# Kernel tuning notes

Hardware: AMD Instinct MI355X
Metric: run time of the kernel (lower is better)

The kernel has to match this reference:

```python
import jax, jax.numpy as jnp
import numpy as np
from jax.scipy.special import digamma, gammaln, logsumexp

N, K, D = 262144, 256, 64
ALPHA = 1.0  # alphaDP
LOG2PI = float(np.log(2.0 * np.pi))


def setup_inputs() -> dict:
    key = jax.random.key(0)
    k1, k2, k3, k4 = jax.random.split(key, 4)
    x = jax.random.normal(k1, (N, D), jnp.float32)
    # variational params (perturbed from the module's init so grads are nontrivial)
    u = 1.0 + jax.random.uniform(k2, (K,), jnp.float32)
    v = 1.0 + jax.random.uniform(k3, (K,), jnp.float32)
    tau = jax.random.normal(k4, (K, D), jnp.float32)
    c = jnp.ones((K,), jnp.float32)
    n = jnp.full((K,), float(D), jnp.float32)   # must be > D-1
    B = jnp.ones((K, D), jnp.float32)
    # fixed prior hyper-parameters (buffers, per init_kwargs)
    tau0 = jnp.zeros((K, D), jnp.float32)
    c0 = jnp.ones((K,), jnp.float32)
    n0 = jnp.full((K,), float(D), jnp.float32)
    B0 = jnp.ones((K, D), jnp.float32)
    return dict(x=x, u=u, v=v, tau=tau, c=c, n=n, B=B,
                tau0=tau0, c0=c0, n0=n0, B0=B0)


def _dpmm_forward(x, u, v, tau, c, n, B, tau0, c0, n0, B0):
    # --- E[log pi_k] from stick-breaking Beta(u_k, v_k) posteriors ---
    dig_sum = digamma(u + v)
    elog_beta = digamma(u) - dig_sum            # (K,)
    elog_1mbeta = digamma(v) - dig_sum          # (K,)
    elog_pi = elog_beta + jnp.concatenate(
        [jnp.zeros((1,), elog_beta.dtype), jnp.cumsum(elog_1mbeta)[:-1]])

    # --- expected Gaussian log-likelihood under diagonal Normal-Wishart q ---
    Elam = n[:, None] / B                                        # (K, D) E[lambda]
    Eloglam = digamma(0.5 * n)[:, None] + jnp.log(2.0) - jnp.log(B)
    # quadratic form sum_d E[lam_kd](x_id - tau_kd)^2 via matmuls (no NxKxD tensor)
    quad = ((x * x) @ Elam.T
            - 2.0 * (x @ (Elam * tau).T)
            + jnp.sum(Elam * tau * tau, axis=-1)[None, :])       # (N, K)
    eloglik = 0.5 * (jnp.sum(Eloglam, axis=-1)[None, :]
                     - D * LOG2PI
                     - (D / c)[None, :]
                     - quad)                                     # (N, K)

    # --- responsibilities ---
    log_rho = elog_pi[None, :] + eloglik                         # (N, K)
    lse = logsumexp(log_rho, axis=-1)                            # (N,)
    pi = jnp.exp(log_rho - lse[:, None])                         # (N, K)

    # --- ELBO: sum_i r_ik (log_rho - log r) = sum_i logsumexp_i, minus KLs ---
    # KL(Beta(u,v) || Beta(1, alpha))
    kl_beta = jnp.sum(gammaln(u + v) - gammaln(u) - gammaln(v)
                      - (gammaln(1.0 + ALPHA) - gammaln(ALPHA))
                      + (u - 1.0) * elog_beta
                      + (v - ALPHA) * elog_1mbeta)
    # KL of diagonal Wishart (per-dim Gamma(n/2, rate=B/2))
    a, a0 = 0.5 * n[:, None], 0.5 * n0[:, None]
    b, b0 = 0.5 * B, 0.5 * B0
    kl_gam = ((a - a0) * digamma(a) - gammaln(a) + gammaln(a0)
              + a0 * (jnp.log(b) - jnp.log(b0)) + a * (b0 - b) / b)  # (K, D)
    # E_lambda KL of conditional Normal(tau, (c lambda)^-1)
    kl_norm = (0.5 * D * (c0 / c - 1.0 + jnp.log(c / c0))
               + 0.5 * c0 * jnp.sum((n[:, None] / B) * (tau - tau0) ** 2, axis=-1))

    elbo = jnp.sum(lse) - kl_beta - jnp.sum(kl_gam) - jnp.sum(kl_norm)
    return pi, elbo


def reference(x, u, v, tau, c, n, B, tau0, c0, n0, B0):
    return _dpmm_forward(x, u, v, tau, c, n, B, tau0, c0, n0, B0)
```

## Files before the change

kernel.cpp:

```cpp
#include <hip/hip_runtime.h>
#include <math.h>
#include <stdint.h>

#define NPTS 262144
#define KCL  256
#define DDIM 64
#define ALPHA_DP 1.0f

#define ROWS_PER_WAVE 32
#define WAVES_PER_BLK 8
#define ROWS_PER_BLK  (ROWS_PER_WAVE * WAVES_PER_BLK)
#define NBLK_MAIN     (NPTS / ROWS_PER_BLK)
#define NPART         (NPTS / ROWS_PER_WAVE)

#define OFF_ELOGPI 32768
#define OFF_BASE   33024
#define OFF_KLB    33280
#define OFF_KLP    33281
#define OFF_PART   33537

#define LN2_F    0.6931471805599453f
#define LOG2PI_F 1.8378770664093453f

typedef _Float16 f16x8  __attribute__((ext_vector_type(8)));
typedef float    f32x4  __attribute__((ext_vector_type(4)));
typedef float    f32x16 __attribute__((ext_vector_type(16)));

__device__ __forceinline__ float digamma_f(float x) {
  float r = 0.0f;
  while (x < 6.0f) { r -= 1.0f / x; x += 1.0f; }
  float inv  = 1.0f / x;
  float inv2 = inv * inv;
  return r + logf(x) - 0.5f * inv
       - inv2 * (0.083333333333333333f
         - inv2 * (0.008333333333333333f
           - inv2 * 0.003968253968253968f));
}

__global__ __launch_bounds__(64) void dpmm_prep(
    const float* __restrict__ u,   const float* __restrict__ v,
    const float* __restrict__ tau, const float* __restrict__ c,
    const float* __restrict__ n,   const float* __restrict__ B,
    const float* __restrict__ tau0, const float* __restrict__ c0,
    const float* __restrict__ n0,  const float* __restrict__ B0,
    float* __restrict__ ws) {
  const int tid = threadIdx.x;

  if (blockIdx.x == KCL) {
    float eb[4], e1b[4], klb[4];
    #pragma unroll
    for (int q = 0; q < 4; ++q) {
      int k = tid * 4 + q;
      float uk = u[k], vk = v[k];
      float ds = digamma_f(uk + vk);
      eb[q]  = digamma_f(uk) - ds;
      e1b[q] = digamma_f(vk) - ds;
      klb[q] = lgammaf(uk + vk) - lgammaf(uk) - lgammaf(vk)
             - (lgammaf(1.0f + ALPHA_DP) - lgammaf(ALPHA_DP))
             + (uk - 1.0f) * eb[q] + (vk - ALPHA_DP) * e1b[q];
    }
    float sum4 = e1b[0] + e1b[1] + e1b[2] + e1b[3];
    float sc = sum4;
    #pragma unroll
    for (int off = 1; off < 64; off <<= 1) {
      float vv = __shfl_up(sc, off, 64);
      if (tid >= off) sc += vv;
    }
    float pre = sc - sum4;
    ws[OFF_ELOGPI + 4 * tid + 0] = eb[0] + pre;  pre += e1b[0];
    ws[OFF_ELOGPI + 4 * tid + 1] = eb[1] + pre;  pre += e1b[1];
    ws[OFF_ELOGPI + 4 * tid + 2] = eb[2] + pre;  pre += e1b[2];
    ws[OFF_ELOGPI + 4 * tid + 3] = eb[3] + pre;
    float ks = klb[0] + klb[1] + klb[2] + klb[3];
    #pragma unroll
    for (int off = 32; off; off >>= 1) ks += __shfl_xor(ks, off, 64);
    if (tid == 0) ws[OFF_KLB] = ks;
    return;
  }

  const int k = blockIdx.x, d = tid;
  _Float16* Wp = (_Float16*)ws;

  float nk = n[k], ck = c[k], n0k = n0[k], c0k = c0[k];
  float Bkd = B[k * DDIM + d],   tkd  = tau[k * DDIM + d];
  float B0kd = B0[k * DDIM + d], t0kd = tau0[k * DDIM + d];
  float Elam = nk / Bkd;
  float wb = Elam * tkd;
  float wa = -0.5f * Elam;

  const int ct = k & 7, col = k >> 3;
  int   kks[2] = { d, 64 + d };
  float wvs[2] = { wb, wa };
  #pragma unroll
  for (int q = 0; q < 2; ++q) {
    int kk = kks[q]; float wq = wvs[q];
    int s = kk >> 4, rem = kk & 15, h = rem >> 3, e = rem & 7;
    int lanei = col + h * 32;
    _Float16 hi = (_Float16)wq, lo = (_Float16)(wq - (float)hi);
    Wp[( s * 8 + ct)     * 512 + lanei * 8 + e] = hi;
    Wp[(64 + s * 8 + ct) * 512 + lanei * 8 + e] = lo;
  }

  float a = 0.5f * nk, a0 = 0.5f * n0k;
  float dga = digamma_f(a);
  float lga = lgammaf(a), lga0 = lgammaf(a0);
  float b = 0.5f * Bkd, b0 = 0.5f * B0kd;
  float klg = (a - a0) * dga - lga + lga0
            + a0 * (logf(b) - logf(b0)) + a * (b0 - b) / b;
  float dt = tkd - t0kd;
  float knq = Elam * dt * dt;
  float negLogB = -logf(Bkd);
  float et2 = Elam * tkd * tkd;

  #pragma unroll
  for (int off = 32; off; off >>= 1) {
    klg     += __shfl_xor(klg, off, 64);
    knq     += __shfl_xor(knq, off, 64);
    negLogB += __shfl_xor(negLogB, off, 64);
    et2     += __shfl_xor(et2, off, 64);
  }
  if (d == 0) {
    float sumEloglam = (float)DDIM * (dga + LN2_F) + negLogB;
    ws[OFF_BASE + k] = 0.5f * (sumEloglam - (float)DDIM * LOG2PI_F
                               - (float)DDIM / ck - et2);
    float kln = 0.5f * (float)DDIM * (c0k / ck - 1.0f + logf(ck / c0k))
              + 0.5f * c0k * knq;
    ws[OFF_KLP + k] = klg + kln;
  }
}

__device__ __forceinline__ void split8(const float* v, f16x8& h, f16x8& l) {
  #pragma unroll
  for (int e = 0; e < 8; ++e) {
    _Float16 hh = (_Float16)v[e];
    h[e] = hh;
    l[e] = (_Float16)(v[e] - (float)hh);
  }
}

__device__ __forceinline__ void gload16(const _Float16* g, _Float16* l) {
  __builtin_amdgcn_global_load_lds(
      reinterpret_cast<const __attribute__((address_space(1))) uint32_t*>(
          reinterpret_cast<uintptr_t>(g)),
      reinterpret_cast<__attribute__((address_space(3))) uint32_t*>(
          reinterpret_cast<uintptr_t>(l)),
      16, 0, 0);
}

__global__ __launch_bounds__(512, 2) void dpmm_mfma(
    const float* __restrict__ x, const _Float16* __restrict__ Wp,
    const float* __restrict__ base, const float* __restrict__ elogpi,
    float* __restrict__ pi, float* __restrict__ partial) {
  __shared__ _Float16 W_sh[2][32768];
  const int tid  = threadIdx.x;
  const int lane = tid & 63;
  const int w    = tid >> 6;
  const int col  = lane & 31;
  const int h    = lane >> 5;

  const long row0 = (long)blockIdx.x * ROWS_PER_BLK + (long)w * ROWS_PER_WAVE;
  const float* xr = x + (row0 + col) * DDIM + h * 8;
  float4 xa[4], xb[4];
  #pragma unroll
  for (int s = 0; s < 4; ++s) {
    xa[s] = *(const float4*)(xr + s * 16);
    xb[s] = *(const float4*)(xr + s * 16 + 4);
  }

  #pragma unroll
  for (int i = 0; i < 8; ++i)
    gload16(Wp + (size_t)(i * 512 + tid) * 8,
            &W_sh[0][(size_t)(i * 512 + w * 64) * 8]);

  f16x8 ah[8], al[8];
  #pragma unroll
  for (int s = 0; s < 4; ++s) {
    float cv[8] = {xa[s].x,xa[s].y,xa[s].z,xa[s].w,xb[s].x,xb[s].y,xb[s].z,xb[s].w};
    float qv[8];
    #pragma unroll
    for (int e = 0; e < 8; ++e) qv[e] = cv[e] * cv[e];
    split8(cv, ah[s], al[s]);
    split8(qv, ah[s + 4], al[s + 4]);
  }

  f32x16 acc[8];
  {
    float4 b0 = *(const float4*)(base + col * 8);
    float4 b1 = *(const float4*)(base + col * 8 + 4);
    float4 e0 = *(const float4*)(elogpi + col * 8);
    float4 e1 = *(const float4*)(elogpi + col * 8 + 4);
    float bb[8] = {b0.x+e0.x, b0.y+e0.y, b0.z+e0.z, b0.w+e0.w,
                   b1.x+e1.x, b1.y+e1.y, b1.z+e1.z, b1.w+e1.w};
    #pragma unroll
    for (int ct = 0; ct < 8; ++ct) {
      #pragma unroll
      for (int j = 0; j < 16; ++j) acc[ct][j] = bb[ct];
    }
  }

  __syncthreads();

  #pragma unroll
  for (int i = 0; i < 8; ++i)
    gload16(Wp + (size_t)(32768 / 8 * 8 + (i * 512 + tid) * 8),
            &W_sh[1][(size_t)(i * 512 + w * 64) * 8]);

  #pragma unroll
  for (int f = 0; f < 64; ++f) {
    const int ss = f >> 3, ct = f & 7;
    f16x8 b = *(const f16x8*)&W_sh[0][(size_t)f * 512 + lane * 8];
    acc[ct] = __builtin_amdgcn_mfma_f32_32x32x16_f16(ah[ss], b, acc[ct], 0, 0, 0);
    acc[ct] = __builtin_amdgcn_mfma_f32_32x32x16_f16(al[ss], b, acc[ct], 0, 0, 0);
  }

  __syncthreads();

  #pragma unroll
  for (int f = 0; f < 64; ++f) {
    const int ss = f >> 3, ct = f & 7;
    f16x8 b = *(const f16x8*)&W_sh[1][(size_t)f * 512 + lane * 8];
    acc[ct] = __builtin_amdgcn_mfma_f32_32x32x16_f16(ah[ss], b, acc[ct], 0, 0, 0);
  }

  float wls = 0.0f;
  #pragma unroll
  for (int j = 0; j < 16; ++j) {
    const int r = (j & 3) + 8 * (j >> 2) + 4 * h;
    float m = acc[0][j];
    #pragma unroll
    for (int ct = 1; ct < 8; ++ct) m = fmaxf(m, acc[ct][j]);
    m = fmaxf(m, __shfl_xor(m, 1, 64));
    m = fmaxf(m, __shfl_xor(m, 2, 64));
    m = fmaxf(m, __shfl_xor(m, 4, 64));
    m = fmaxf(m, __shfl_xor(m, 8, 64));
    m = fmaxf(m, __shfl_xor(m, 16, 64));
    float ev[8]; float s = 0.0f;
    #pragma unroll
    for (int ct = 0; ct < 8; ++ct) { ev[ct] = __expf(acc[ct][j] - m); s += ev[ct]; }
    s += __shfl_xor(s, 1, 64);
    s += __shfl_xor(s, 2, 64);
    s += __shfl_xor(s, 4, 64);
    s += __shfl_xor(s, 8, 64);
    s += __shfl_xor(s, 16, 64);
    float rs = 1.0f / s;
    float* pr = pi + (size_t)(row0 + r) * KCL + col * 8;
    f32x4 p0 = { ev[0]*rs, ev[1]*rs, ev[2]*rs, ev[3]*rs };
    f32x4 p1 = { ev[4]*rs, ev[5]*rs, ev[6]*rs, ev[7]*rs };
    *(f32x4*)(pr + 0) = p0;
    *(f32x4*)(pr + 4) = p1;
    wls += m + __logf(s);
  }
  wls += __shfl_xor(wls, 1, 64);
  wls += __shfl_xor(wls, 2, 64);
  wls += __shfl_xor(wls, 4, 64);
  wls += __shfl_xor(wls, 8, 64);
  wls += __shfl_xor(wls, 16, 64);
  wls += __shfl_xor(wls, 32, 64);
  if (lane == 0) partial[blockIdx.x * WAVES_PER_BLK + w] = wls * 0.03125f;
}

__global__ void dpmm_fin(const float* __restrict__ ws,
                         float* __restrict__ out_elbo) {
  __shared__ double red[256];
  const int t = threadIdx.x;
  double s = 0.0;
  for (int i = t; i < NPART; i += 256) s += (double)ws[OFF_PART + i];
  s -= (double)ws[OFF_KLP + t];
  red[t] = s;
  __syncthreads();
  for (int off = 128; off; off >>= 1) {
    if (t < off) red[t] += red[t + off];
    __syncthreads();
  }
  if (t == 0) out_elbo[0] = (float)(red[0] - (double)ws[OFF_KLB]);
}

extern "C" void kernel_launch(void* const* d_in, const int* in_sizes, int n_in,
                              void* d_out, int out_size, void* d_ws, size_t ws_size,
                              hipStream_t stream) {
  const float* x    = (const float*)d_in[0];
  const float* u    = (const float*)d_in[1];
  const float* v    = (const float*)d_in[2];
  const float* tau  = (const float*)d_in[3];
  const float* c    = (const float*)d_in[4];
  const float* n    = (const float*)d_in[5];
  const float* B    = (const float*)d_in[6];
  const float* tau0 = (const float*)d_in[7];
  const float* c0   = (const float*)d_in[8];
  const float* n0   = (const float*)d_in[9];
  const float* B0   = (const float*)d_in[10];

  float* out = (float*)d_out;
  float* ws  = (float*)d_ws;

  dpmm_prep<<<KCL + 1, 64, 0, stream>>>(u, v, tau, c, n, B, tau0, c0, n0, B0, ws);

  const _Float16* Wp  = (const _Float16*)ws;
  const float* base   = ws + OFF_BASE;
  const float* elogpi = ws + OFF_ELOGPI;
  float* partial      = ws + OFF_PART;

  dpmm_mfma<<<NBLK_MAIN, 512, 0, stream>>>(x, Wp, base, elogpi, out, partial);
  dpmm_fin<<<1, 256, 0, stream>>>(ws, out + (size_t)NPTS * KCL);
}
```

Baseline: 123.3 us.

## Split cluster columns across wave pairs and stream weights in small double-buffered chunks

```diff
diff --git a/kernel.cpp b/kernel.cpp
--- a/kernel.cpp
+++ b/kernel.cpp
@@ -7,11 +7,9 @@
 #define DDIM 64
 #define ALPHA_DP 1.0f
 
-#define ROWS_PER_WAVE 32
-#define WAVES_PER_BLK 8
-#define ROWS_PER_BLK  (ROWS_PER_WAVE * WAVES_PER_BLK)
+#define ROWS_PER_BLK  64
 #define NBLK_MAIN     (NPTS / ROWS_PER_BLK)
-#define NPART         (NPTS / ROWS_PER_WAVE)
+#define NPART         (NPTS / 32)
 
 #define OFF_ELOGPI 32768
 #define OFF_BASE   33024
@@ -147,18 +145,21 @@
       16, 0, 0);
 }
 
-__global__ __launch_bounds__(512, 2) void dpmm_mfma(
+__global__ __launch_bounds__(256, 3) void dpmm_mfma(
     const float* __restrict__ x, const _Float16* __restrict__ Wp,
     const float* __restrict__ base, const float* __restrict__ elogpi,
     float* __restrict__ pi, float* __restrict__ partial) {
-  __shared__ _Float16 W_sh[2][32768];
+  __shared__ _Float16 W_sh[2][8192];
+  __shared__ float ex_m[2][64], ex_s[2][64];
   const int tid  = threadIdx.x;
   const int lane = tid & 63;
   const int w    = tid >> 6;
+  const int rg   = w & 1;
+  const int q    = w >> 1;
   const int col  = lane & 31;
   const int h    = lane >> 5;
 
-  const long row0 = (long)blockIdx.x * ROWS_PER_BLK + (long)w * ROWS_PER_WAVE;
+  const long row0 = (long)blockIdx.x * ROWS_PER_BLK + (long)rg * 32;
   const float* xr = x + (row0 + col) * DDIM + h * 8;
   float4 xa[4], xb[4];
   #pragma unroll
@@ -168,9 +169,8 @@
   }
 
   #pragma unroll
-  for (int i = 0; i < 8; ++i)
-    gload16(Wp + (size_t)(i * 512 + tid) * 8,
-            &W_sh[0][(size_t)(i * 512 + w * 64) * 8]);
+  for (int i = 0; i < 4; ++i)
+    gload16(Wp + (size_t)(i * 256 + tid) * 8, &W_sh[0][(i * 256 + w * 64) * 8]);
 
   f16x8 ah[8], al[8];
   #pragma unroll
@@ -183,80 +183,89 @@
     split8(qv, ah[s + 4], al[s + 4]);
   }
 
-  f32x16 acc[8];
+  f32x16 acc[4];
   {
-    float4 b0 = *(const float4*)(base + col * 8);
-    float4 b1 = *(const float4*)(base + col * 8 + 4);
-    float4 e0 = *(const float4*)(elogpi + col * 8);
-    float4 e1 = *(const float4*)(elogpi + col * 8 + 4);
-    float bb[8] = {b0.x+e0.x, b0.y+e0.y, b0.z+e0.z, b0.w+e0.w,
-                   b1.x+e1.x, b1.y+e1.y, b1.z+e1.z, b1.w+e1.w};
-    #pragma unroll
-    for (int ct = 0; ct < 8; ++ct) {
+    float4 b0 = *(const float4*)(base + col * 8 + 4 * q);
+    float4 e0 = *(const float4*)(elogpi + col * 8 + 4 * q);
+    float bb[4] = {b0.x+e0.x, b0.y+e0.y, b0.z+e0.z, b0.w+e0.w};
+    #pragma unroll
+    for (int t4 = 0; t4 < 4; ++t4) {
       #pragma unroll
-      for (int j = 0; j < 16; ++j) acc[ct][j] = bb[ct];
+      for (int j = 0; j < 16; ++j) acc[t4][j] = bb[t4];
     }
   }
 
   __syncthreads();
 
   #pragma unroll
-  for (int i = 0; i < 8; ++i)
-    gload16(Wp + (size_t)(32768 / 8 * 8 + (i * 512 + tid) * 8),
-            &W_sh[1][(size_t)(i * 512 + w * 64) * 8]);
-
-  #pragma unroll
-  for (int f = 0; f < 64; ++f) {
-    const int ss = f >> 3, ct = f & 7;
-    f16x8 b = *(const f16x8*)&W_sh[0][(size_t)f * 512 + lane * 8];
-    acc[ct] = __builtin_amdgcn_mfma_f32_32x32x16_f16(ah[ss], b, acc[ct], 0, 0, 0);
-    acc[ct] = __builtin_amdgcn_mfma_f32_32x32x16_f16(al[ss], b, acc[ct], 0, 0, 0);
-  }
-
-  __syncthreads();
-
-  #pragma unroll
-  for (int f = 0; f < 64; ++f) {
-    const int ss = f >> 3, ct = f & 7;
-    f16x8 b = *(const f16x8*)&W_sh[1][(size_t)f * 512 + lane * 8];
-    acc[ct] = __builtin_amdgcn_mfma_f32_32x32x16_f16(ah[ss], b, acc[ct], 0, 0, 0);
-  }
-
-  float wls = 0.0f;
+  for (int c = 0; c < 8; ++c) {
+    if (c + 1 < 8) {
+      #pragma unroll
+      for (int i = 0; i < 4; ++i)
+        gload16(Wp + (size_t)(c + 1) * 8192 + (size_t)(i * 256 + tid) * 8,
+                &W_sh[(c + 1) & 1][(i * 256 + w * 64) * 8]);
+    }
+    const _Float16* Ws = W_sh[c & 1];
+    const int sbase = (c < 4) ? 2 * c : 2 * (c - 4);
+    #pragma unroll
+    for (int sl = 0; sl < 2; ++sl) {
+      const int s = sbase + sl;
+      #pragma unroll
+      for (int t4 = 0; t4 < 4; ++t4) {
+        const int lfi = sl * 8 + 4 * q + t4;
+        f16x8 b = *(const f16x8*)&Ws[(size_t)lfi * 512 + lane * 8];
+        acc[t4] = __builtin_amdgcn_mfma_f32_32x32x16_f16(ah[s], b, acc[t4], 0, 0, 0);
+        if (c < 4)
+          acc[t4] = __builtin_amdgcn_mfma_f32_32x32x16_f16(al[s], b, acc[t4], 0, 0, 0);
+      }
+    }
+    if (c + 1 < 8) __syncthreads();
+  }
+
   #pragma unroll
   for (int j = 0; j < 16; ++j) {
     const int r = (j & 3) + 8 * (j >> 2) + 4 * h;
-    float m = acc[0][j];
-    #pragma unroll
-    for (int ct = 1; ct < 8; ++ct) m = fmaxf(m, acc[ct][j]);
+    float m = fmaxf(fmaxf(acc[0][j], acc[1][j]), fmaxf(acc[2][j], acc[3][j]));
     m = fmaxf(m, __shfl_xor(m, 1, 64));
     m = fmaxf(m, __shfl_xor(m, 2, 64));
     m = fmaxf(m, __shfl_xor(m, 4, 64));
     m = fmaxf(m, __shfl_xor(m, 8, 64));
     m = fmaxf(m, __shfl_xor(m, 16, 64));
-    float ev[8]; float s = 0.0f;
-    #pragma unroll
-    for (int ct = 0; ct < 8; ++ct) { ev[ct] = __expf(acc[ct][j] - m); s += ev[ct]; }
+    float s = __expf(acc[0][j] - m) + __expf(acc[1][j] - m)
+            + __expf(acc[2][j] - m) + __expf(acc[3][j] - m);
     s += __shfl_xor(s, 1, 64);
     s += __shfl_xor(s, 2, 64);
     s += __shfl_xor(s, 4, 64);
     s += __shfl_xor(s, 8, 64);
     s += __shfl_xor(s, 16, 64);
-    float rs = 1.0f / s;
-    float* pr = pi + (size_t)(row0 + r) * KCL + col * 8;
-    f32x4 p0 = { ev[0]*rs, ev[1]*rs, ev[2]*rs, ev[3]*rs };
-    f32x4 p1 = { ev[4]*rs, ev[5]*rs, ev[6]*rs, ev[7]*rs };
-    *(f32x4*)(pr + 0) = p0;
-    *(f32x4*)(pr + 4) = p1;
-    wls += m + __logf(s);
-  }
-  wls += __shfl_xor(wls, 1, 64);
-  wls += __shfl_xor(wls, 2, 64);
-  wls += __shfl_xor(wls, 4, 64);
-  wls += __shfl_xor(wls, 8, 64);
-  wls += __shfl_xor(wls, 16, 64);
-  wls += __shfl_xor(wls, 32, 64);
-  if (lane == 0) partial[blockIdx.x * WAVES_PER_BLK + w] = wls * 0.03125f;
+    if (col == 0) { ex_m[q][rg * 32 + r] = m; ex_s[q][rg * 32 + r] = s; }
+  }
+  __syncthreads();
+
+  float wls = 0.0f;
+  #pragma unroll
+  for (int j = 0; j < 16; ++j) {
+    const int r = (j & 3) + 8 * (j >> 2) + 4 * h;
+    const int rb = rg * 32 + r;
+    float m1 = ex_m[0][rb], s1 = ex_s[0][rb];
+    float m2 = ex_m[1][rb], s2 = ex_s[1][rb];
+    float gm = fmaxf(m1, m2);
+    float gs = s1 * __expf(m1 - gm) + s2 * __expf(m2 - gm);
+    float rs = 1.0f / gs;
+    f32x4 pv = { __expf(acc[0][j] - gm) * rs, __expf(acc[1][j] - gm) * rs,
+                 __expf(acc[2][j] - gm) * rs, __expf(acc[3][j] - gm) * rs };
+    *(f32x4*)(pi + (size_t)(row0 + r) * KCL + col * 8 + 4 * q) = pv;
+    wls += gm + __logf(gs);
+  }
+  if (q == 0) {
+    wls += __shfl_xor(wls, 1, 64);
+    wls += __shfl_xor(wls, 2, 64);
+    wls += __shfl_xor(wls, 4, 64);
+    wls += __shfl_xor(wls, 8, 64);
+    wls += __shfl_xor(wls, 16, 64);
+    wls += __shfl_xor(wls, 32, 64);
+    if (lane == 0) partial[blockIdx.x * 2 + rg] = wls * 0.03125f;
+  }
 }
 
 __global__ void dpmm_fin(const float* __restrict__ ws,
@@ -300,6 +309,6 @@
   const float* elogpi = ws + OFF_ELOGPI;
   float* partial      = ws + OFF_PART;
 
-  dpmm_mfma<<<NBLK_MAIN, 512, 0, stream>>>(x, Wp, base, elogpi, out, partial);
+  dpmm_mfma<<<NBLK_MAIN, 256, 0, stream>>>(x, Wp, base, elogpi, out, partial);
   dpmm_fin<<<1, 256, 0, stream>>>(ws, out + (size_t)NPTS * KCL);
 }
```

After: 158.8 us. +28.8%, slower.
